# Kernel optimization log

Measured on AMD Instinct MI355X. Metric: run time of the kernel, lower is better.

## Reference

```python
import jax, jax.numpy as jnp
import numpy as np

VOCAB = 50257
EMBED = 1024

def setup_inputs() -> dict:
    key = jax.random.key(0)
    k1, k2 = jax.random.split(key)
    hidden_states = jax.random.normal(k1, (2, 2048, EMBED), dtype=jnp.float32)
    # nn.Linear weight: [vocab_size, embed_dim], no bias
    W = jax.random.normal(k2, (VOCAB, EMBED), dtype=jnp.float32) * (1.0 / np.sqrt(EMBED))
    return {"hidden_states": hidden_states, "W": W}

def reference(hidden_states, W):
    # logits: [B, S, V] = hidden @ W^T
    logits = jnp.einsum("bsd,vd->bsv", hidden_states, W)
    return jax.nn.log_softmax(logits, axis=-1)
```

## Files before the change

kernel.cpp:

```cpp
#include <hip/hip_runtime.h>
#include <hip/hip_bf16.h>
#include <math.h>

#define VOCAB 50257
#define VPAD  50432
#define EMB   1024
#define NROWS 4096

#define BM 256
#define BN 256
#define BK 64
#define NKT (EMB / BK)
#define NMT (NROWS / BM)
#define NT  (VPAD / BN)
#define NWG (NMT * NT)

typedef __attribute__((ext_vector_type(4))) float  f32x4;
typedef __attribute__((ext_vector_type(4), aligned(4))) float f32x4u;
typedef __attribute__((ext_vector_type(4))) __bf16 bf16x4;
typedef __attribute__((ext_vector_type(8))) __bf16 bf16x8;

#define FENCE asm volatile("" ::: "memory")
#define BARRIER do { FENCE; __builtin_amdgcn_s_barrier(); FENCE; } while (0)

__global__ __launch_bounds__(256)
void cvt_bf16(const float* __restrict__ src, __bf16* __restrict__ dst,
              long n_src, long n_dst) {
    long i = ((long)blockIdx.x * 256 + threadIdx.x) * 8;
    if (i >= n_dst) return;
    bf16x8 o;
    if (i < n_src) {
        f32x4 a = *(const f32x4*)(src + i);
        f32x4 b = *(const f32x4*)(src + i + 4);
        #pragma unroll
        for (int e = 0; e < 4; ++e) {
            o[e]     = (__bf16)a[e];
            o[4 + e] = (__bf16)b[e];
        }
    } else {
        #pragma unroll
        for (int e = 0; e < 8; ++e) o[e] = (__bf16)0.0f;
    }
    *(bf16x8*)(dst + i) = o;
}

template <bool LB_OUT>
__global__ __launch_bounds__(512, 2)
void gemm_fused(const __bf16* __restrict__ A, const __bf16* __restrict__ B,
                float* __restrict__ C, __bf16* __restrict__ Lb,
                float* __restrict__ pbuf) {
    __shared__ alignas(16) __bf16 S[65536];

    const int tid  = threadIdx.x;
    const int lane = tid & 63;
    const int wave = tid >> 6;
    const int wm   = (wave >> 2) * 128;
    const int wn   = (wave & 3) * 64;
    const int frow = lane & 15;
    const int hi   = lane >> 4;

    const int b  = blockIdx.x;
    const int lg = (b & 7) * (NWG / 8) + (b >> 3);
    const int q  = lg >> 4, w = lg & 15;
    int mt, nt;
    if (q == 196) { mt = w; nt = 196; }
    else { mt = (q & 1) * 8 + (w & 7); nt = (q >> 1) * 2 + (w >> 3); }
    const int mtB = mt * BM, ntB = nt * BN;

    const int r0 = tid >> 3;
    const int ls = (tid & 7) ^ (r0 & 7);
    const __bf16* gA = A + (size_t)(mtB + r0) * EMB + ls * 8;
    const __bf16* gB = B + (size_t)(ntB + r0) * EMB + ls * 8;

    f32x4 acc[8][4];
    const f32x4 vzero = {0.f, 0.f, 0.f, 0.f};
    #pragma unroll
    for (int m = 0; m < 8; ++m)
        #pragma unroll
        for (int n = 0; n < 4; ++n) acc[m][n] = vzero;

#define STAGE_UNIT(bc, kt, u) do {                                            \
        const __bf16* g_ = ((u) < 2 ? gB : gA) + ((size_t)(((u)&1) * 128) * EMB + (kt) * BK); \
        __bf16* d_ = &S[(bc) * 32768 + ((u) < 2 ? 16384 : 0) + ((u)&1) * 8192 + wave * 512]; \
        __builtin_amdgcn_global_load_lds(                                     \
            (const __attribute__((address_space(1))) void*)g_,               \
            (__attribute__((address_space(3))) void*)d_, 16, 0, 0);          \
        __builtin_amdgcn_global_load_lds(                                     \
            (const __attribute__((address_space(1))) void*)(g_ + (size_t)64 * EMB), \
            (__attribute__((address_space(3))) void*)(d_ + 4096), 16, 0, 0); \
    } while (0)

#define LDA_TO(dst, c, mh, ks) { _Pragma("unroll")                            \
    for (int i_ = 0; i_ < 4; ++i_) {                                          \
        const int row_ = wm + ((mh) * 4 + i_) * 16 + frow;                    \
        dst[i_] = *(const bf16x8*)&S[(c) * 32768 + row_ * 64 + ((((ks) * 4 + hi)) ^ (row_ & 7)) * 8]; } }

#define LDB_TO(dst, c, ks) { _Pragma("unroll")                                \
    for (int n_ = 0; n_ < 4; ++n_) {                                          \
        const int row_ = wn + n_ * 16 + frow;                                 \
        dst[n_] = *(const bf16x8*)&S[(c) * 32768 + 16384 + row_ * 64 + ((((ks) * 4 + hi)) ^ (row_ & 7)) * 8]; } }

#define MFMA16(mh, AF, BF)                                                    \
    __builtin_amdgcn_s_setprio(1);                                            \
    _Pragma("unroll") for (int i_ = 0; i_ < 4; ++i_)                          \
        _Pragma("unroll") for (int n_ = 0; n_ < 4; ++n_)                      \
            acc[(mh) * 4 + i_][n_] = __builtin_amdgcn_mfma_f32_16x16x32_bf16( \
                AF[i_], BF[n_], acc[(mh) * 4 + i_][n_], 0, 0, 0);             \
    __builtin_amdgcn_s_setprio(0);

    bf16x8 afA[4], afB[4], bfrA[4], bfrB[4];

    #pragma unroll
    for (int u = 0; u < 4; ++u) STAGE_UNIT(0, 0, u);

    #pragma unroll 2
    for (int t = 0; t < NKT; ++t) {
        const int c = t & 1;
        const bool pf = (t + 1 < NKT);
        if (pf) {
            STAGE_UNIT(c ^ 1, t + 1, 0);
            STAGE_UNIT(c ^ 1, t + 1, 1);
            asm volatile("s_waitcnt vmcnt(4)" ::: "memory");
        } else {
            asm volatile("s_waitcnt vmcnt(0)" ::: "memory");
        }
        BARRIER;
        LDB_TO(bfrA, c, 0);
        LDA_TO(afA, c, 0, 0);
        LDA_TO(afB, c, 1, 0);
        MFMA16(0, afA, bfrA);
        if (pf) STAGE_UNIT(c ^ 1, t + 1, 2);
        LDB_TO(bfrB, c, 1);
        LDA_TO(afA, c, 0, 1);
        MFMA16(1, afB, bfrA);
        if (pf) STAGE_UNIT(c ^ 1, t + 1, 3);
        LDA_TO(afB, c, 1, 1);
        MFMA16(0, afA, bfrB);
        MFMA16(1, afB, bfrB);
        BARRIER;
    }
#undef STAGE_UNIT

    __syncthreads();
    const bool edge = (ntB + BN > VOCAB);

    if (LB_OUT) {
        #pragma unroll
        for (int m = 0; m < 8; ++m) {
            const size_t rbase = (size_t)(mtB + wm + m * 16 + hi * 4) * VPAD;
            #pragma unroll
            for (int n = 0; n < 4; ++n) {
                const size_t col = ntB + wn + n * 16 + frow;
                #pragma unroll
                for (int r = 0; r < 4; ++r)
                    Lb[rbase + (size_t)r * VPAD + col] = (__bf16)acc[m][n][r];
            }
        }
    } else {
        #pragma unroll
        for (int m = 0; m < 8; ++m) {
            const size_t rbase = (size_t)(mtB + wm + m * 16 + hi * 4) * VOCAB;
            #pragma unroll
            for (int n = 0; n < 4; ++n) {
                const int col = ntB + wn + n * 16 + frow;
                if (!edge || col < VOCAB) {
                    #pragma unroll
                    for (int r = 0; r < 4; ++r)
                        C[rbase + (size_t)r * VOCAB + col] = acc[m][n][r];
                }
            }
        }
    }

    float* ldsP = (float*)&S[0];
    const int lcid = (wave & 3) * 16 + frow;
    #pragma unroll
    for (int m = 0; m < 8; ++m) {
        #pragma unroll
        for (int r = 0; r < 4; ++r) {
            float s = 0.0f;
            #pragma unroll
            for (int n = 0; n < 4; ++n) {
                if (!edge || (ntB + wn + n * 16 + frow) < VOCAB)
                    s += __expf(acc[m][n][r]);
            }
            ldsP[(wm + m * 16 + hi * 4 + r) * 68 + lcid] = s;
        }
    }
    __syncthreads();

    {
        const int rl = tid >> 1, hf = tid & 1;
        const float* q2 = ldsP + rl * 68 + hf * 32;
        float s = 0.0f;
        #pragma unroll
        for (int k = 0; k < 8; ++k) {
            f32x4 v = *(const f32x4*)(q2 + k * 4);
            s += v[0] + v[1] + v[2] + v[3];
        }
        s += __shfl_xor(s, 1);
        if (hf == 0) pbuf[(size_t)nt * NROWS + mtB + rl] = s;
    }
}

__global__ __launch_bounds__(256)
void lse_reduce(const float* __restrict__ pbuf, float* __restrict__ lse) {
    __shared__ float sl[4][64];
    const int r0 = blockIdx.x * 64;
    const int l  = threadIdx.x & 63;
    const int w  = threadIdx.x >> 6;
    float s = 0.0f;
    for (int t = w; t < NT; t += 4)
        s += pbuf[(size_t)t * NROWS + r0 + l];
    sl[w][l] = s;
    __syncthreads();
    if (threadIdx.x < 64)
        lse[r0 + l] = __logf(sl[0][l] + sl[1][l] + sl[2][l] + sl[3][l]);
}

__global__ __launch_bounds__(256)
void expand_sub(const __bf16* __restrict__ Lb, const float* __restrict__ lse,
                float* __restrict__ C) {
    const int row = blockIdx.x >> 2;
    const int q   = blockIdx.x & 3;
    const float s = lse[row];
    const __bf16* src = Lb + (size_t)row * VPAD;
    float* dst = C + (size_t)row * VOCAB;
    const int i0 = q * 1571;
    const int i1 = (q == 3) ? 6282 : i0 + 1571;
    for (int i = i0 + threadIdx.x; i < i1; i += 256) {
        bf16x8 v = __builtin_nontemporal_load((const bf16x8*)(src + i * 8));
        f32x4u a, b2;
        a[0] = (float)v[0] - s; a[1] = (float)v[1] - s;
        a[2] = (float)v[2] - s; a[3] = (float)v[3] - s;
        b2[0] = (float)v[4] - s; b2[1] = (float)v[5] - s;
        b2[2] = (float)v[6] - s; b2[3] = (float)v[7] - s;
        __builtin_nontemporal_store(a,  (f32x4u*)(dst + i * 8));
        __builtin_nontemporal_store(b2, (f32x4u*)(dst + i * 8 + 4));
    }
    if (q == 3 && threadIdx.x == 0)
        dst[50256] = (float)src[50256] - s;
}

__global__ __launch_bounds__(256)
void sub_lse(float* __restrict__ C, const float* __restrict__ lse) {
    const int row = blockIdx.x;
    const float s = lse[row];
    float* p = C + (size_t)row * VOCAB;
    for (int i = threadIdx.x; i < 12564; i += 256) {
        f32x4u v = *(const f32x4u*)(p + 4 * i);
        v[0] -= s; v[1] -= s; v[2] -= s; v[3] -= s;
        *(f32x4u*)(p + 4 * i) = v;
    }
    if (threadIdx.x == 0) p[50256] -= s;
}

#define FBM 128
#define FBK 32
__device__ __forceinline__ int swz_idx(int row, int col) {
    int slot = (col >> 3) ^ ((row >> 1) & 3);
    return row * FBK + slot * 8 + (col & 7);
}

__global__ __launch_bounds__(256, 2)
void gemm_logits(const float* __restrict__ H, const float* __restrict__ W,
                 float* __restrict__ C) {
    __shared__ __bf16 ldsA[FBM * FBK];
    __shared__ __bf16 ldsB[FBM * FBK];

    const int tid  = threadIdx.x;
    const int lane = tid & 63;
    const int wave = tid >> 6;
    const int wm = (wave >> 1) * 64;
    const int wn = (wave & 1) * 64;
    const int mt = blockIdx.x;
    const int nt = blockIdx.y;
    const int srow = tid >> 1;
    const int scol = (tid & 1) * 16;
    const int brow_g = nt * FBM + srow;
    const bool bvalid = brow_g < VOCAB;
    const float* aptr = H + (size_t)(mt * FBM + srow) * EMB + scol;
    const float* bptr = W + (size_t)(bvalid ? brow_g : 0) * EMB + scol;

    f32x4 areg[4], breg[4];
    #pragma unroll
    for (int q = 0; q < 4; ++q) {
        areg[q] = *(const f32x4*)(aptr + q * 4);
        breg[q] = *(const f32x4*)(bptr + q * 4);
    }
    f32x4 acc[4][4];
    const f32x4 vzero = {0.f, 0.f, 0.f, 0.f};
    #pragma unroll
    for (int i = 0; i < 4; ++i)
        #pragma unroll
        for (int j = 0; j < 4; ++j) acc[i][j] = vzero;

    const int frow = lane & 15;
    const int kcol = (lane >> 4) * 8;

    for (int kt = 0; kt < EMB / FBK; ++kt) {
        __syncthreads();
        #pragma unroll
        for (int q = 0; q < 4; ++q) {
            const int col = scol + q * 4;
            bf16x4 av, bv;
            #pragma unroll
            for (int e = 0; e < 4; ++e) {
                av[e] = (__bf16)areg[q][e];
                bv[e] = bvalid ? (__bf16)breg[q][e] : (__bf16)0.0f;
            }
            *(bf16x4*)(&ldsA[swz_idx(srow, col)]) = av;
            *(bf16x4*)(&ldsB[swz_idx(srow, col)]) = bv;
        }
        __syncthreads();
        if (kt + 1 < EMB / FBK) {
            const int ko = (kt + 1) * FBK;
            #pragma unroll
            for (int q = 0; q < 4; ++q) {
                areg[q] = *(const f32x4*)(aptr + ko + q * 4);
                breg[q] = *(const f32x4*)(bptr + ko + q * 4);
            }
        }
        bf16x8 af[4], bfr[4];
        #pragma unroll
        for (int i = 0; i < 4; ++i) {
            af[i]  = *(const bf16x8*)(&ldsA[swz_idx(wm + i * 16 + frow, kcol)]);
            bfr[i] = *(const bf16x8*)(&ldsB[swz_idx(wn + i * 16 + frow, kcol)]);
        }
        #pragma unroll
        for (int i = 0; i < 4; ++i)
            #pragma unroll
            for (int j = 0; j < 4; ++j)
                acc[i][j] = __builtin_amdgcn_mfma_f32_16x16x32_bf16(
                    af[i], bfr[j], acc[i][j], 0, 0, 0);
    }

    const int crow = mt * FBM + wm + (lane >> 4) * 4;
    const int ccol = nt * FBM + wn + (lane & 15);
    #pragma unroll
    for (int i = 0; i < 4; ++i) {
        #pragma unroll
        for (int j = 0; j < 4; ++j) {
            const int col = ccol + j * 16;
            if (col < VOCAB) {
                #pragma unroll
                for (int r = 0; r < 4; ++r)
                    C[(size_t)(crow + i * 16 + r) * VOCAB + col] = acc[i][j][r];
            }
        }
    }
}

__global__ __launch_bounds__(256)
void row_lse(const float* __restrict__ C, float* __restrict__ lse) {
    const int row = blockIdx.x;
    const float* p = C + (size_t)row * VOCAB;

    float m = -INFINITY, l = 0.0f;
    for (int i = threadIdx.x; i < 12564; i += 256) {
        f32x4u v = *(const f32x4u*)(p + 4 * i);
        #pragma unroll
        for (int e = 0; e < 4; ++e) {
            const float x  = v[e];
            const float mn = fmaxf(m, x);
            l = l * __expf(m - mn) + __expf(x - mn);
            m = mn;
        }
    }
    if (threadIdx.x == 0) {
        const float x  = p[50256];
        const float mn = fmaxf(m, x);
        l = l * __expf(m - mn) + __expf(x - mn);
        m = mn;
    }
    #pragma unroll
    for (int off = 1; off < 64; off <<= 1) {
        const float mo = __shfl_xor(m, off);
        const float lo = __shfl_xor(l, off);
        const float mn = fmaxf(m, mo);
        l = l * __expf(m - mn) + lo * __expf(mo - mn);
        m = mn;
    }
    __shared__ float sm[4], sl[4];
    if ((threadIdx.x & 63) == 0) { sm[threadIdx.x >> 6] = m; sl[threadIdx.x >> 6] = l; }
    __syncthreads();
    if (threadIdx.x == 0) {
        m = sm[0]; l = sl[0];
        #pragma unroll
        for (int w = 1; w < 4; ++w) {
            const float mn = fmaxf(m, sm[w]);
            l = l * __expf(m - mn) + sl[w] * __expf(sm[w] - mn);
            m = mn;
        }
        lse[row] = m + __logf(l);
    }
}

extern "C" void kernel_launch(void* const* d_in, const int* in_sizes, int n_in,
                              void* d_out, int out_size, void* d_ws, size_t ws_size,
                              hipStream_t stream) {
    const float* H = (const float*)d_in[0];
    const float* W = (const float*)d_in[1];
    float* C   = (float*)d_out;
    float* lse = (float*)d_ws;

    const long nH  = (long)NROWS * EMB;
    const long nW  = (long)VOCAB * EMB;
    const long nWp = (long)VPAD * EMB;

    const size_t pb_off   = 16384;
    const size_t pb_bytes = (size_t)NT * NROWS * sizeof(float);
    const size_t hb_off   = (pb_off + pb_bytes + 255) & ~(size_t)255;
    const size_t wb_off   = hb_off + (size_t)nH * 2;
    const size_t lb_off   = wb_off + (size_t)nWp * 2;
    const size_t lb_bytes = (size_t)NROWS * VPAD * 2;
    const size_t need_lb   = lb_off + lb_bytes;
    const size_t need_full = lb_off;

    if (ws_size >= need_full) {
        __bf16* Hb = (__bf16*)((char*)d_ws + hb_off);
        __bf16* Wb = (__bf16*)((char*)d_ws + wb_off);
        float*  pb = (float*)((char*)d_ws + pb_off);
        cvt_bf16<<<(int)(nH / 8 / 256), 256, 0, stream>>>(H, Hb, nH, nH);
        cvt_bf16<<<(int)((nWp / 8 + 255) / 256), 256, 0, stream>>>(W, Wb, nW, nWp);
        if (ws_size >= need_lb) {
            __bf16* Lb = (__bf16*)((char*)d_ws + lb_off);
            gemm_fused<true><<<dim3(NWG), 512, 0, stream>>>(Hb, Wb, C, Lb, pb);
            lse_reduce<<<dim3(NROWS / 64), 256, 0, stream>>>(pb, lse);
            expand_sub<<<dim3(NROWS * 4), 256, 0, stream>>>(Lb, lse, C);
        } else {
            gemm_fused<false><<<dim3(NWG), 512, 0, stream>>>(Hb, Wb, C, (__bf16*)nullptr, pb);
            lse_reduce<<<dim3(NROWS / 64), 256, 0, stream>>>(pb, lse);
            sub_lse<<<dim3(NROWS), 256, 0, stream>>>(C, lse);
        }
    } else {
        dim3 ggrid(NROWS / FBM, (VOCAB + FBM - 1) / FBM);
        gemm_logits<<<ggrid, 256, 0, stream>>>(H, W, C);
        row_lse<<<dim3(NROWS), 256, 0, stream>>>(C, lse);
        sub_lse<<<dim3(NROWS), 256, 0, stream>>>(C, lse);
    }
}
```

Measured before the change: 787.4 us.

## Switch GEMM inner loop from 16x16x32 to 32x32x16 bf16 MFMA tiles

Replaces the 16x16x32 MFMA fragments with 32x32x16 MFMAs. Each wave now computes its 128x64 tile as 4x2 blocks of 32x32 with 16-float accumulators, and the LDS fragment loads, epilogue stores and row-sum reduction are remapped to the new accumulator layout. The larger MFMA shape reads fewer LDS fragments per flop and issues fewer MFMA instructions. In exchange it adds an extra cross-lane shuffle in the exp-sum epilogue, and the new store pattern and register pressure may hurt.

```diff
diff --git a/kernel.cpp b/kernel.cpp
--- a/kernel.cpp
+++ b/kernel.cpp
@@ -16,6 +16,7 @@
 #define NWG (NMT * NT)
 
 typedef __attribute__((ext_vector_type(4))) float  f32x4;
+typedef __attribute__((ext_vector_type(16))) float f32x16;
 typedef __attribute__((ext_vector_type(4), aligned(4))) float f32x4u;
 typedef __attribute__((ext_vector_type(4))) __bf16 bf16x4;
 typedef __attribute__((ext_vector_type(8))) __bf16 bf16x8;
@@ -56,8 +57,8 @@
     const int wave = tid >> 6;
     const int wm   = (wave >> 2) * 128;
     const int wn   = (wave & 3) * 64;
-    const int frow = lane & 15;
-    const int hi   = lane >> 4;
+    const int l31  = lane & 31;
+    const int h    = lane >> 5;
 
     const int b  = blockIdx.x;
     const int lg = (b & 7) * (NWG / 8) + (b >> 3);
@@ -72,12 +73,13 @@
     const __bf16* gA = A + (size_t)(mtB + r0) * EMB + ls * 8;
     const __bf16* gB = B + (size_t)(ntB + r0) * EMB + ls * 8;
 
-    f32x4 acc[8][4];
-    const f32x4 vzero = {0.f, 0.f, 0.f, 0.f};
-    #pragma unroll
-    for (int m = 0; m < 8; ++m)
-        #pragma unroll
-        for (int n = 0; n < 4; ++n) acc[m][n] = vzero;
+    f32x16 acc[4][2];
+    #pragma unroll
+    for (int mb = 0; mb < 4; ++mb)
+        #pragma unroll
+        for (int nb = 0; nb < 2; ++nb)
+            #pragma unroll
+            for (int e = 0; e < 16; ++e) acc[mb][nb][e] = 0.0f;
 
 #define STAGE_UNIT(bc, kt, u) do {                                            \
         const __bf16* g_ = ((u) < 2 ? gB : gA) + ((size_t)(((u)&1) * 128) * EMB + (kt) * BK); \
@@ -90,25 +92,25 @@
             (__attribute__((address_space(3))) void*)(d_ + 4096), 16, 0, 0); \
     } while (0)
 
-#define LDA_TO(dst, c, mh, ks) { _Pragma("unroll")                            \
-    for (int i_ = 0; i_ < 4; ++i_) {                                          \
-        const int row_ = wm + ((mh) * 4 + i_) * 16 + frow;                    \
-        dst[i_] = *(const bf16x8*)&S[(c) * 32768 + row_ * 64 + ((((ks) * 4 + hi)) ^ (row_ & 7)) * 8]; } }
-
-#define LDB_TO(dst, c, ks) { _Pragma("unroll")                                \
-    for (int n_ = 0; n_ < 4; ++n_) {                                          \
-        const int row_ = wn + n_ * 16 + frow;                                 \
-        dst[n_] = *(const bf16x8*)&S[(c) * 32768 + 16384 + row_ * 64 + ((((ks) * 4 + hi)) ^ (row_ & 7)) * 8]; } }
-
-#define MFMA16(mh, AF, BF)                                                    \
+#define LDA32(dst, c, ks) { _Pragma("unroll")                                 \
+    for (int mb_ = 0; mb_ < 4; ++mb_) {                                       \
+        const int row_ = wm + mb_ * 32 + l31;                                 \
+        dst[mb_] = *(const bf16x8*)&S[(c) * 32768 + row_ * 64 + ((((ks) * 2 + h)) ^ (row_ & 7)) * 8]; } }
+
+#define LDB32(dst, c, ks) { _Pragma("unroll")                                 \
+    for (int nb_ = 0; nb_ < 2; ++nb_) {                                       \
+        const int row_ = wn + nb_ * 32 + l31;                                 \
+        dst[nb_] = *(const bf16x8*)&S[(c) * 32768 + 16384 + row_ * 64 + ((((ks) * 2 + h)) ^ (row_ & 7)) * 8]; } }
+
+#define MFMA8(AF, BF)                                                         \
     __builtin_amdgcn_s_setprio(1);                                            \
-    _Pragma("unroll") for (int i_ = 0; i_ < 4; ++i_)                          \
-        _Pragma("unroll") for (int n_ = 0; n_ < 4; ++n_)                      \
-            acc[(mh) * 4 + i_][n_] = __builtin_amdgcn_mfma_f32_16x16x32_bf16( \
-                AF[i_], BF[n_], acc[(mh) * 4 + i_][n_], 0, 0, 0);             \
+    _Pragma("unroll") for (int mb_ = 0; mb_ < 4; ++mb_)                       \
+        _Pragma("unroll") for (int nb_ = 0; nb_ < 2; ++nb_)                   \
+            acc[mb_][nb_] = __builtin_amdgcn_mfma_f32_32x32x16_bf16(          \
+                AF[mb_], BF[nb_], acc[mb_][nb_], 0, 0, 0);                    \
     __builtin_amdgcn_s_setprio(0);
 
-    bf16x8 afA[4], afB[4], bfrA[4], bfrB[4];
+    bf16x8 afA[4], afB[4], bfrA[2], bfrB[2];
 
     #pragma unroll
     for (int u = 0; u < 4; ++u) STAGE_UNIT(0, 0, u);
@@ -125,18 +127,16 @@
             asm volatile("s_waitcnt vmcnt(0)" ::: "memory");
         }
         BARRIER;
-        LDB_TO(bfrA, c, 0);
-        LDA_TO(afA, c, 0, 0);
-        LDA_TO(afB, c, 1, 0);
-        MFMA16(0, afA, bfrA);
+        LDB32(bfrA, c, 0); LDA32(afA, c, 0);
+        LDB32(bfrB, c, 1); LDA32(afB, c, 1);
+        MFMA8(afA, bfrA);
         if (pf) STAGE_UNIT(c ^ 1, t + 1, 2);
-        LDB_TO(bfrB, c, 1);
-        LDA_TO(afA, c, 0, 1);
-        MFMA16(1, afB, bfrA);
+        LDB32(bfrA, c, 2); LDA32(afA, c, 2);
+        MFMA8(afB, bfrB);
         if (pf) STAGE_UNIT(c ^ 1, t + 1, 3);
-        LDA_TO(afB, c, 1, 1);
-        MFMA16(0, afA, bfrB);
-        MFMA16(1, afB, bfrB);
+        LDB32(bfrB, c, 3); LDA32(afB, c, 3);
+        MFMA8(afA, bfrA);
+        MFMA8(afB, bfrB);
         BARRIER;
     }
 #undef STAGE_UNIT
@@ -146,45 +146,43 @@
 
     if (LB_OUT) {
         #pragma unroll
-        for (int m = 0; m < 8; ++m) {
-            const size_t rbase = (size_t)(mtB + wm + m * 16 + hi * 4) * VPAD;
-            #pragma unroll
-            for (int n = 0; n < 4; ++n) {
-                const size_t col = ntB + wn + n * 16 + frow;
-                #pragma unroll
-                for (int r = 0; r < 4; ++r)
-                    Lb[rbase + (size_t)r * VPAD + col] = (__bf16)acc[m][n][r];
+        for (int mb = 0; mb < 4; ++mb) {
+            #pragma unroll
+            for (int r = 0; r < 16; ++r) {
+                const int grow = mtB + wm + mb * 32 + (r & 3) + 8 * (r >> 2) + 4 * h;
+                const size_t rb = (size_t)grow * VPAD + ntB + wn + l31;
+                Lb[rb]      = (__bf16)acc[mb][0][r];
+                Lb[rb + 32] = (__bf16)acc[mb][1][r];
             }
         }
     } else {
         #pragma unroll
-        for (int m = 0; m < 8; ++m) {
-            const size_t rbase = (size_t)(mtB + wm + m * 16 + hi * 4) * VOCAB;
-            #pragma unroll
-            for (int n = 0; n < 4; ++n) {
-                const int col = ntB + wn + n * 16 + frow;
-                if (!edge || col < VOCAB) {
-                    #pragma unroll
-                    for (int r = 0; r < 4; ++r)
-                        C[rbase + (size_t)r * VOCAB + col] = acc[m][n][r];
-                }
+        for (int mb = 0; mb < 4; ++mb) {
+            #pragma unroll
+            for (int r = 0; r < 16; ++r) {
+                const int grow = mtB + wm + mb * 32 + (r & 3) + 8 * (r >> 2) + 4 * h;
+                const size_t rb = (size_t)grow * VOCAB;
+                const int col0 = ntB + wn + l31;
+                if (!edge || col0 < VOCAB)      C[rb + col0]      = acc[mb][0][r];
+                if (!edge || col0 + 32 < VOCAB) C[rb + col0 + 32] = acc[mb][1][r];
             }
         }
     }
 
     float* ldsP = (float*)&S[0];
-    const int lcid = (wave & 3) * 16 + frow;
-    #pragma unroll
-    for (int m = 0; m < 8; ++m) {
-        #pragma unroll
-        for (int r = 0; r < 4; ++r) {
+    const int col0 = ntB + wn + l31;
+    #pragma unroll
+    for (int mb = 0; mb < 4; ++mb) {
+        #pragma unroll
+        for (int r = 0; r < 16; ++r) {
             float s = 0.0f;
-            #pragma unroll
-            for (int n = 0; n < 4; ++n) {
-                if (!edge || (ntB + wn + n * 16 + frow) < VOCAB)
-                    s += __expf(acc[m][n][r]);
-            }
-            ldsP[(wm + m * 16 + hi * 4 + r) * 68 + lcid] = s;
+            if (!edge || col0 < VOCAB)      s += __expf(acc[mb][0][r]);
+            if (!edge || col0 + 32 < VOCAB) s += __expf(acc[mb][1][r]);
+            s += __shfl_xor(s, 16);
+            if (l31 < 16) {
+                const int lrow = wm + mb * 32 + (r & 3) + 8 * (r >> 2) + 4 * h;
+                ldsP[lrow * 68 + (wave & 3) * 16 + (lane & 15)] = s;
+            }
         }
     }
     __syncthreads();
```

After: 829.6 us. +5.4%, slower.
